# Performance work log

Measured on AMD Instinct MI355X. Metric: run time of the kernel, lower is better.

Reference implementation:

```python
import jax, jax.numpy as jnp
import numpy as np

NUM_STEPS = 3
NUM_HEADS = 8
HEAD_DIM = 128
EPS = 1e-5


def layernorm(x, g, b):
    mu = jnp.mean(x, -1, keepdims=True)
    var = jnp.mean(jnp.square(x - mu), -1, keepdims=True)
    return (x - mu) * jax.lax.rsqrt(var + EPS) * g + b


def entmax15(x):
    # Exact entmax-1.5 along last axis (Peters & Martins 2019, sort-based).
    x = (x - jnp.max(x, -1, keepdims=True)) / 2.0
    xs = jnp.flip(jnp.sort(x, -1), -1)  # descending sort
    rho = jnp.arange(1, x.shape[-1] + 1, dtype=x.dtype)
    mean = jnp.cumsum(xs, -1) / rho
    meansq = jnp.cumsum(xs * xs, -1) / rho
    ss = rho * (meansq - jnp.square(mean))
    tau = mean - jnp.sqrt(jnp.clip((1.0 - ss) / rho, 0.0, None))
    support = jnp.sum(tau <= xs, -1, keepdims=True)
    tau_star = jnp.take_along_axis(tau, support - 1, -1)
    return jnp.square(jnp.clip(x - tau_star, 0.0, None))


def setup_inputs() -> dict:
    key = jax.random.key(0)
    ks = jax.random.split(key, 6)
    B, S, Hd, Md, N = 2, 1024, 2048, 1024, 2048
    THD = NUM_HEADS * HEAD_DIM
    return {
        "hidden": jax.random.normal(ks[0], (B, S, Hd), jnp.float32),
        "memory": jax.random.normal(ks[1], (N, Md), jnp.float32),
        "Wq": jax.random.normal(ks[2], (THD, Hd), jnp.float32) / np.float32(np.sqrt(Hd)),
        "Wk": jax.random.normal(ks[3], (THD, Md), jnp.float32) / np.float32(np.sqrt(Md)),
        "Wv": jax.random.normal(ks[4], (THD, Md), jnp.float32) / np.float32(np.sqrt(Md)),
        "Wo": jax.random.normal(ks[5], (Hd, THD), jnp.float32) / np.float32(np.sqrt(THD)),
        "log_beta": jnp.full((NUM_HEADS,), float(np.log(1.0 / np.sqrt(HEAD_DIM))), jnp.float32),
        "g_state": jnp.ones((Hd,), jnp.float32),
        "b_state": jnp.zeros((Hd,), jnp.float32),
        "g_mem": jnp.ones((Md,), jnp.float32),
        "b_mem": jnp.zeros((Md,), jnp.float32),
    }


def reference(hidden, memory, Wq, Wk, Wv, Wo, log_beta, g_state, b_state, g_mem, b_mem):
    B, S, _ = hidden.shape
    N = memory.shape[0]
    H, hd = NUM_HEADS, HEAD_DIM
    # projections
    Q = layernorm(hidden, g_state, b_state) @ Wq.T            # (B,S,H*hd)
    mn = layernorm(memory, g_mem, b_mem)                      # (N,Md)
    K = (mn @ Wk.T).reshape(N, H, hd).transpose(1, 0, 2)      # (H,N,hd)
    V = (mn @ Wv.T).reshape(N, H, hd).transpose(1, 0, 2)      # (H,N,hd)
    xi = Q.reshape(B, S, H, hd).transpose(0, 2, 1, 3)          # (B,H,S,hd)
    beta = jnp.exp(log_beta)[None, :, None, None]
    for _ in range(NUM_STEPS):
        scores = jnp.einsum('bhsd,hnd->bhsn', xi, K) * beta    # (B,H,S,N)
        w = entmax15(scores)
        xi = jnp.einsum('bhsn,hnd->bhsd', w, V)
    out = xi.transpose(0, 2, 1, 3).reshape(B, S, H * hd) @ Wo.T  # (B,S,hidden_dim)
    return out
```

## Files before the change

### kernel.cpp

```cpp
#include <hip/hip_runtime.h>

typedef _Float16 half8 __attribute__((ext_vector_type(8)));
typedef _Float16 hv4 __attribute__((ext_vector_type(4)));
typedef float fv4 __attribute__((ext_vector_type(4)));

typedef __attribute__((address_space(3))) unsigned lds_u32;
typedef const __attribute__((address_space(1))) unsigned glb_u32;

__device__ __forceinline__ void gll16(const void* g, void* l) {
  __builtin_amdgcn_global_load_lds((glb_u32*)g, (lds_u32*)l, 16, 0, 0);
}

__global__ __launch_bounds__(256) void ln_rows(const float* __restrict__ in,
                                               const float* __restrict__ g,
                                               const float* __restrict__ bb,
                                               _Float16* __restrict__ out, int ncols) {
  __shared__ float sm[8];
  int row = blockIdx.x, t = threadIdx.x;
  const float* rp = in + (size_t)row * ncols;
  int nv = ncols >> 10;
  fv4 v[2];
  float s1 = 0.f, s2 = 0.f;
#pragma unroll
  for (int c = 0; c < 2; ++c)
    if (c < nv) {
      v[c] = *(const fv4*)(rp + c * 1024 + t * 4);
#pragma unroll
      for (int j = 0; j < 4; ++j) { s1 += v[c][j]; s2 += v[c][j] * v[c][j]; }
    }
#pragma unroll
  for (int off = 32; off > 0; off >>= 1) { s1 += __shfl_xor(s1, off, 64); s2 += __shfl_xor(s2, off, 64); }
  int w = t >> 6;
  if ((t & 63) == 0) { sm[w] = s1; sm[4 + w] = s2; }
  __syncthreads();
  s1 = sm[0] + sm[1] + sm[2] + sm[3];
  s2 = sm[4] + sm[5] + sm[6] + sm[7];
  float inv = 1.0f / (float)ncols;
  float mu = s1 * inv;
  float var = s2 * inv - mu * mu;
  float rstd = rsqrtf(var + 1e-5f);
#pragma unroll
  for (int c = 0; c < 2; ++c)
    if (c < nv) {
      int col = c * 1024 + t * 4;
      fv4 gg = *(const fv4*)(g + col);
      fv4 bv = *(const fv4*)(bb + col);
      hv4 o;
#pragma unroll
      for (int j = 0; j < 4; ++j) o[j] = (_Float16)(((v[c][j] - mu) * rstd) * gg[j] + bv[j]);
      *(hv4*)(out + (size_t)row * ncols + col) = o;
    }
}

__global__ __launch_bounds__(256) void cast_f16(const float* __restrict__ in,
                                                _Float16* __restrict__ out, int n) {
  int i = (blockIdx.x * 256 + threadIdx.x) << 2;
  if (i < n) {
    fv4 f = *(const fv4*)(in + i);
    hv4 h;
#pragma unroll
    for (int j = 0; j < 4; ++j) h[j] = (_Float16)f[j];
    *(hv4*)(out + i) = h;
  }
}

__global__ __launch_bounds__(256) void reduce_split(const float* __restrict__ parts, int ns,
                                                    long long stride,
                                                    _Float16* __restrict__ hi, int n) {
  int i = (blockIdx.x * 256 + threadIdx.x) << 2;
  if (i < n) {
    fv4 s = *(const fv4*)(parts + i);
    for (int j = 1; j < ns; ++j) {
      fv4 v = *(const fv4*)(parts + (size_t)j * stride + i);
      s += v;
    }
    hv4 h;
#pragma unroll
    for (int j = 0; j < 4; ++j) h[j] = (_Float16)s[j];
    *(hv4*)(hi + i) = h;
  }
}

__global__ __launch_bounds__(256) void entmax_c(const _Float16* __restrict__ scores,
                                                float* __restrict__ crow) {
  __shared__ float comp[4][512];
  int wid = threadIdx.x >> 6;
  int row = blockIdx.x * 4 + wid;
  int l = threadIdx.x & 63;
  unsigned long long lmask = (1ull << l) - 1ull;
  const half8* sp = (const half8*)(scores + (size_t)row * 2048);
  half8 hx[4];
#pragma unroll
  for (int i = 0; i < 4; ++i) hx[i] = sp[i * 64 + l];
  fv4 x[8];
#pragma unroll
  for (int i = 0; i < 4; ++i)
#pragma unroll
    for (int j = 0; j < 8; ++j) x[i * 2 + (j >> 2)][j & 3] = (float)hx[i][j];
  float m = x[0][0];
#pragma unroll
  for (int i = 0; i < 8; ++i)
#pragma unroll
    for (int j = 0; j < 4; ++j) m = fmaxf(m, x[i][j]);
#pragma unroll
  for (int off = 32; off > 0; off >>= 1) m = fmaxf(m, __shfl_xor(m, off, 64));
#pragma unroll
  for (int i = 0; i < 8; ++i)
#pragma unroll
    for (int j = 0; j < 4; ++j) x[i][j] = (x[i][j] - m) * 0.5f;

  float tau = -1.0f;
  bool fixed = false;
  int cnti = 2048;
  for (int it = 0; it < 6 && !fixed; ++it) {
    float s1 = 0.f, s2 = 0.f;
    cnti = 0;
#pragma unroll
    for (int i = 0; i < 8; ++i)
#pragma unroll
      for (int j = 0; j < 4; ++j) {
        bool a = x[i][j] > tau;
        cnti += (int)__builtin_popcountll(__ballot(a));
        float sel = a ? x[i][j] : 0.f;
        s1 += sel;
        s2 = fmaf(sel, sel, s2);
      }
#pragma unroll
    for (int off = 32; off > 0; off >>= 1) {
      s1 += __shfl_xor(s1, off, 64);
      s2 += __shfl_xor(s2, off, 64);
    }
    float cnt = (float)cnti;
    float mean = s1 / cnt;
    float ss = s2 - s1 * mean;
    float nt = mean - sqrtf(fmaxf((1.0f - ss) / cnt, 0.0f));
    if (nt == tau) fixed = true;
    else tau = nt;
    if (cnti <= 512) break;
  }
  if (!fixed) {
    if (cnti <= 512) {
      int base = 0;
#pragma unroll
      for (int i = 0; i < 8; ++i)
#pragma unroll
        for (int j = 0; j < 4; ++j) {
          bool a = x[i][j] > tau;
          unsigned long long mk = __ballot(a);
          if (a) comp[wid][base + (int)__builtin_popcountll(mk & lmask)] = x[i][j];
          base += (int)__builtin_popcountll(mk);
        }
      float y[8];
#pragma unroll
      for (int r = 0; r < 8; ++r) {
        int idx = r * 64 + l;
        y[r] = (idx < base) ? comp[wid][idx] : -2.0f;
      }
      for (int it = 0; it < 10 && !fixed; ++it) {
        float s1 = 0.f, s2 = 0.f;
        int c = 0;
#pragma unroll
        for (int r = 0; r < 8; ++r) {
          bool a = y[r] > tau;
          c += (int)__builtin_popcountll(__ballot(a));
          float sel = a ? y[r] : 0.f;
          s1 += sel;
          s2 = fmaf(sel, sel, s2);
        }
#pragma unroll
        for (int off = 32; off > 0; off >>= 1) {
          s1 += __shfl_xor(s1, off, 64);
          s2 += __shfl_xor(s2, off, 64);
        }
        float cnt = (float)c;
        float mean = s1 / cnt;
        float ss = s2 - s1 * mean;
        float nt = mean - sqrtf(fmaxf((1.0f - ss) / cnt, 0.0f));
        if (nt == tau) fixed = true;
        else tau = nt;
      }
    } else {
      for (int it = 0; it < 8 && !fixed; ++it) {
        float s1 = 0.f, s2 = 0.f;
        int c = 0;
#pragma unroll
        for (int i = 0; i < 8; ++i)
#pragma unroll
          for (int j = 0; j < 4; ++j) {
            bool a = x[i][j] > tau;
            c += (int)__builtin_popcountll(__ballot(a));
            float sel = a ? x[i][j] : 0.f;
            s1 += sel;
            s2 = fmaf(sel, sel, s2);
          }
#pragma unroll
        for (int off = 32; off > 0; off >>= 1) {
          s1 += __shfl_xor(s1, off, 64);
          s2 += __shfl_xor(s2, off, 64);
        }
        float cnt = (float)c;
        float mean = s1 / cnt;
        float ss = s2 - s1 * mean;
        float nt = mean - sqrtf(fmaxf((1.0f - ss) / cnt, 0.0f));
        if (nt == tau) fixed = true;
        else tau = nt;
      }
    }
  }

  if (l == 0) crow[row] = 0.5f * m + tau;
}

struct GemmParams {
  const _Float16 *A, *B, *B2;
  const float* crow;
  _Float16 *C16, *C16b;
  float* C32;
  const float* log_beta;
  int K, lda, ldb;
  long long aSB, aSH, bSH;
  long long crowSB, crowSH;
  long long cSB, cSH, cOsR, cOsC;
  long long cOsRb, cOsCb;
  long long partStride;
  int alphaMode, outMode, outModeB, nsplit, dual;
};

template <int AMODE>
__global__ __launch_bounds__(256) void gemm_nt(GemmParams p) {
  constexpr int AST = AMODE ? 40 : 32;
  __shared__ __align__(16) _Float16 As[128 * AST];
  __shared__ __align__(16) _Float16 Bs[128 * 32];
  int t = threadIdx.x;
  int m0 = blockIdx.y * 128;
  int bx = blockIdx.x, n0, kbeg, kend, ks = 0;
  if (p.nsplit > 1) {
    ks = bx % p.nsplit;
    n0 = (bx / p.nsplit) * 128;
    int kl = p.K / p.nsplit;
    kbeg = ks * kl;
    kend = kbeg + kl;
  } else {
    n0 = bx * 128;
    kbeg = 0;
    kend = p.K;
  }
  int z = blockIdx.z, bidx, h, job = 0;
  if (p.dual) { job = z; bidx = 0; h = 0; }
  else { bidx = z >> 3; h = z & 7; }
  const _Float16* pA = p.A + bidx * p.aSB + h * p.aSH;
  const _Float16* pB = (job ? p.B2 : p.B) + h * p.bSH;
  const float* pc = AMODE ? p.crow + bidx * p.crowSB + h * p.crowSH : nullptr;

  fv4 acc[4][4] = {};
  int wv = t >> 6, l = t & 63, quad = l >> 4, lr = l & 15;
  int wm = (wv >> 1) * 64, wn = (wv & 1) * 64;
  int rl = l >> 2, cl = (l & 3) * 8;

  for (int k0 = kbeg; k0 < kend; k0 += 32) {
#pragma unroll
    for (int v = 0; v < 2; ++v) {
      int rb = wv * 16 + v * 64;
      int r = rb + rl;
      size_t aOff = (size_t)(m0 + r) * p.lda + k0 + cl;
      size_t bOff = (size_t)(n0 + r) * p.ldb + k0 + cl;
      if (AMODE == 0) {
        gll16(pA + aOff, &As[rb * 32]);
      } else {
        half8 s8 = *(const half8*)(pA + aOff);
        _Float16 c0 = (_Float16)pc[m0 + r];
        half8 d = s8 * (_Float16)0.5f - c0;
        d = __builtin_elementwise_max(d, (half8)(0));
        half8 w8 = d * d;
        *(half8*)&As[r * AST + cl] = w8;
      }
      gll16(pB + bOff, &Bs[rb * 32]);
    }
    __syncthreads();
    half8 ah[4], bh[4];
#pragma unroll
    for (int mi = 0; mi < 4; ++mi) ah[mi] = *(const half8*)&As[(wm + mi * 16 + lr) * AST + quad * 8];
#pragma unroll
    for (int ni = 0; ni < 4; ++ni) bh[ni] = *(const half8*)&Bs[(wn + ni * 16 + lr) * 32 + quad * 8];
#pragma unroll
    for (int mi = 0; mi < 4; ++mi)
#pragma unroll
      for (int ni = 0; ni < 4; ++ni)
        acc[mi][ni] = __builtin_amdgcn_mfma_f32_16x16x32_f16(ah[mi], bh[ni], acc[mi][ni], 0, 0, 0);
    __syncthreads();
  }

  float alpha = p.alphaMode ? __expf(p.log_beta[h]) : 1.0f;
  int om = (p.dual && job) ? p.outModeB : p.outMode;
  _Float16* c16 = (p.dual && job) ? p.C16b : p.C16;
  long long osR = (p.dual && job) ? p.cOsRb : p.cOsR;
  long long osC = (p.dual && job) ? p.cOsCb : p.cOsC;
  float* c32 = p.C32 + (p.nsplit > 1 ? (long long)ks * p.partStride : 0);
  long long cOff = (long long)bidx * p.cSB + (long long)h * p.cSH;
#pragma unroll
  for (int mi = 0; mi < 4; ++mi)
#pragma unroll
    for (int ni = 0; ni < 4; ++ni) {
      int row = m0 + wm + mi * 16 + quad * 4;
      int col = n0 + wn + ni * 16 + lr;
#pragma unroll
      for (int r = 0; r < 4; ++r) {
        float val = acc[mi][ni][r] * alpha;
        long long idx = cOff + (long long)(row + r) * osR + (long long)col * osC;
        if (om == 1) c32[idx] = val;
        else c16[idx] = (_Float16)val;
      }
    }
}

extern "C" void kernel_launch(void* const* d_in, const int* in_sizes, int n_in,
                              void* d_out, int out_size, void* d_ws, size_t ws_size,
                              hipStream_t stream) {
  const float* hidden = (const float*)d_in[0];
  const float* memory = (const float*)d_in[1];
  const float* Wq = (const float*)d_in[2];
  const float* Wk = (const float*)d_in[3];
  const float* Wv = (const float*)d_in[4];
  const float* Wo = (const float*)d_in[5];
  const float* log_beta = (const float*)d_in[6];
  const float* g_state = (const float*)d_in[7];
  const float* b_state = (const float*)d_in[8];
  const float* g_mem = (const float*)d_in[9];
  const float* b_mem = (const float*)d_in[10];

  char* w = (char*)d_ws;
  auto alloc = [&](size_t bytes) {
    char* r = w;
    w += (bytes + 255) & ~(size_t)255;
    return r;
  };
  _Float16* wq16 = (_Float16*)alloc(2097152 * 2);
  _Float16* wk16 = (_Float16*)alloc(1048576 * 2);
  _Float16* wv16 = (_Float16*)alloc(1048576 * 2);
  _Float16* wo16 = (_Float16*)alloc(2097152 * 2);
  _Float16* lnh16 = (_Float16*)alloc(4194304 * 2);
  _Float16* mn16 = (_Float16*)alloc(2097152 * 2);
  _Float16* kph = (_Float16*)alloc(2097152 * 2);
  _Float16* vt16 = (_Float16*)alloc(2097152 * 2);
  _Float16* xih = (_Float16*)alloc(2097152 * 2);
  float* parts = (float*)alloc((size_t)8 * 2097152 * 4);
  _Float16* scores16 = (_Float16*)alloc((size_t)33554432 * 2);
  float* crow = (float*)alloc(16384 * 4);

  ln_rows<<<2048, 256, 0, stream>>>(hidden, g_state, b_state, lnh16, 2048);
  ln_rows<<<2048, 256, 0, stream>>>(memory, g_mem, b_mem, mn16, 1024);
  cast_f16<<<2048, 256, 0, stream>>>(Wq, wq16, 2097152);
  cast_f16<<<1024, 256, 0, stream>>>(Wk, wk16, 1048576);
  cast_f16<<<1024, 256, 0, stream>>>(Wv, wv16, 1048576);
  cast_f16<<<2048, 256, 0, stream>>>(Wo, wo16, 2097152);

  {
    GemmParams p{};
    p.A = lnh16; p.lda = 2048;
    p.B = wq16; p.ldb = 2048;
    p.K = 2048; p.nsplit = 2;
    p.C32 = parts; p.outMode = 1; p.partStride = 2097152;
    p.cOsR = 1024; p.cOsC = 1;
    gemm_nt<0><<<dim3(16, 16, 1), 256, 0, stream>>>(p);
    reduce_split<<<2048, 256, 0, stream>>>(parts, 2, 2097152, xih, 2097152);
  }
  {
    GemmParams p{};
    p.A = mn16; p.lda = 1024;
    p.B = wk16; p.B2 = wv16; p.ldb = 1024;
    p.K = 1024; p.dual = 1;
    p.C16 = kph; p.outMode = 0; p.cOsR = 1024; p.cOsC = 1;
    p.C16b = vt16; p.outModeB = 0; p.cOsRb = 1; p.cOsCb = 2048;
    gemm_nt<0><<<dim3(8, 16, 2), 256, 0, stream>>>(p);
  }

  for (int step = 0; step < 3; ++step) {
    {
      GemmParams p{};
      p.A = xih;
      p.lda = 1024; p.aSB = 1048576; p.aSH = 128;
      p.B = kph; p.ldb = 1024; p.bSH = 128;
      p.K = 128;
      p.alphaMode = 1; p.log_beta = log_beta;
      p.C16 = scores16; p.outMode = 0;
      p.cSB = 16777216; p.cSH = 2097152;
      p.cOsR = 2048; p.cOsC = 1;
      gemm_nt<0><<<dim3(16, 8, 16), 256, 0, stream>>>(p);
    }
    entmax_c<<<4096, 256, 0, stream>>>(scores16, crow);
    {
      GemmParams p{};
      p.A = scores16; p.crow = crow;
      p.lda = 2048; p.aSB = 16777216; p.aSH = 2097152;
      p.crowSB = 8192; p.crowSH = 1024;
      p.B = vt16; p.ldb = 2048; p.bSH = 262144;
      p.K = 2048; p.nsplit = 4;
      p.C32 = parts; p.outMode = 1; p.partStride = 2097152;
      p.cSB = 1048576; p.cSH = 128;
      p.cOsR = 1024; p.cOsC = 1;
      gemm_nt<1><<<dim3(4, 8, 16), 256, 0, stream>>>(p);
    }
    reduce_split<<<2048, 256, 0, stream>>>(parts, 4, 2097152, xih, 2097152);
  }

  {
    GemmParams p{};
    p.A = xih; p.lda = 1024;
    p.B = wo16; p.ldb = 1024;
    p.K = 1024;
    p.C32 = (float*)d_out; p.outMode = 1;
    p.cOsR = 2048; p.cOsC = 1;
    gemm_nt<0><<<dim3(16, 16, 1), 256, 0, stream>>>(p);
  }
}
```

Measured before the change: 478.8 us.

## Fuse scores, entmax and weighted-value GEMM into one per-step kernel

Each Hopfield step now runs as one kernel, hop_step. A block takes 16 query rows of one head, computes scaled scores with MFMA into LDS, solves the entmax threshold per row in LDS, and multiplies the entmax weights by V to write xi directly. This removes the large fp16 scores buffer in global memory and its repeated write and read, the crow buffer, the split-K partials and the reduce kernel. In exchange, every block streams the whole K and V head slices straight from global memory without LDS staging, so those loads rely heavily on cache. The roughly 74 KB of LDS per block also limits occupancy.

```diff
diff --git a/kernel.cpp b/kernel.cpp
--- a/kernel.cpp
+++ b/kernel.cpp
@@ -81,155 +81,203 @@
   }
 }
 
-__global__ __launch_bounds__(256) void entmax_c(const _Float16* __restrict__ scores,
-                                                float* __restrict__ crow) {
+#define SST 2056
+__global__ __launch_bounds__(256, 2) void hop_step(const _Float16* __restrict__ xi,
+                                                   const _Float16* __restrict__ kp,
+                                                   const _Float16* __restrict__ vt,
+                                                   const float* __restrict__ log_beta,
+                                                   _Float16* __restrict__ xout) {
+  __shared__ __align__(16) _Float16 Ss[16 * SST];
   __shared__ float comp[4][512];
-  int wid = threadIdx.x >> 6;
-  int row = blockIdx.x * 4 + wid;
-  int l = threadIdx.x & 63;
+  __shared__ float cs[16];
+  int strip = blockIdx.x, h = blockIdx.y, b = blockIdx.z;
+  int t = threadIdx.x, wv = t >> 6, l = t & 63;
+  int quad = l >> 4, lr = l & 15;
   unsigned long long lmask = (1ull << l) - 1ull;
-  const half8* sp = (const half8*)(scores + (size_t)row * 2048);
-  half8 hx[4];
-#pragma unroll
-  for (int i = 0; i < 4; ++i) hx[i] = sp[i * 64 + l];
-  fv4 x[8];
-#pragma unroll
-  for (int i = 0; i < 4; ++i)
-#pragma unroll
-    for (int j = 0; j < 8; ++j) x[i * 2 + (j >> 2)][j & 3] = (float)hx[i][j];
-  float m = x[0][0];
-#pragma unroll
-  for (int i = 0; i < 8; ++i)
-#pragma unroll
-    for (int j = 0; j < 4; ++j) m = fmaxf(m, x[i][j]);
-#pragma unroll
-  for (int off = 32; off > 0; off >>= 1) m = fmaxf(m, __shfl_xor(m, off, 64));
-#pragma unroll
-  for (int i = 0; i < 8; ++i)
-#pragma unroll
-    for (int j = 0; j < 4; ++j) x[i][j] = (x[i][j] - m) * 0.5f;
-
-  float tau = -1.0f;
-  bool fixed = false;
-  int cnti = 2048;
-  for (int it = 0; it < 6 && !fixed; ++it) {
-    float s1 = 0.f, s2 = 0.f;
-    cnti = 0;
+  float beta = __expf(log_beta[h]);
+
+  const _Float16* xiA = xi + ((size_t)(b * 1024 + strip * 16)) * 1024 + h * 128;
+  const _Float16* Kb = kp + h * 128;
+  const _Float16* Vb = vt + (size_t)h * 128 * 2048;
+
+  half8 af[4];
+#pragma unroll
+  for (int ki = 0; ki < 4; ++ki)
+    af[ki] = *(const half8*)(xiA + (size_t)lr * 1024 + ki * 32 + quad * 8);
+  for (int nt = wv * 32; nt < wv * 32 + 32; ++nt) {
+    int n0 = nt * 16;
+    fv4 acc = {};
+#pragma unroll
+    for (int ki = 0; ki < 4; ++ki) {
+      half8 bf = *(const half8*)(Kb + (size_t)(n0 + lr) * 1024 + ki * 32 + quad * 8);
+      acc = __builtin_amdgcn_mfma_f32_16x16x32_f16(af[ki], bf, acc, 0, 0, 0);
+    }
+#pragma unroll
+    for (int r = 0; r < 4; ++r)
+      Ss[(quad * 4 + r) * SST + n0 + lr] = (_Float16)(acc[r] * beta);
+  }
+  __syncthreads();
+
+  for (int rr = 0; rr < 4; ++rr) {
+    int row = wv * 4 + rr;
+    const half8* rp = (const half8*)&Ss[row * SST];
+    half8 hx[4];
+#pragma unroll
+    for (int i = 0; i < 4; ++i) hx[i] = rp[i * 64 + l];
+    fv4 x[8];
+#pragma unroll
+    for (int i = 0; i < 4; ++i)
+#pragma unroll
+      for (int j = 0; j < 8; ++j) x[i * 2 + (j >> 2)][j & 3] = (float)hx[i][j];
+    float m = x[0][0];
 #pragma unroll
     for (int i = 0; i < 8; ++i)
 #pragma unroll
-      for (int j = 0; j < 4; ++j) {
-        bool a = x[i][j] > tau;
-        cnti += (int)__builtin_popcountll(__ballot(a));
-        float sel = a ? x[i][j] : 0.f;
-        s1 += sel;
-        s2 = fmaf(sel, sel, s2);
-      }
-#pragma unroll
-    for (int off = 32; off > 0; off >>= 1) {
-      s1 += __shfl_xor(s1, off, 64);
-      s2 += __shfl_xor(s2, off, 64);
-    }
-    float cnt = (float)cnti;
-    float mean = s1 / cnt;
-    float ss = s2 - s1 * mean;
-    float nt = mean - sqrtf(fmaxf((1.0f - ss) / cnt, 0.0f));
-    if (nt == tau) fixed = true;
-    else tau = nt;
-    if (cnti <= 512) break;
-  }
-  if (!fixed) {
-    if (cnti <= 512) {
-      int base = 0;
+      for (int j = 0; j < 4; ++j) m = fmaxf(m, x[i][j]);
+#pragma unroll
+    for (int off = 32; off > 0; off >>= 1) m = fmaxf(m, __shfl_xor(m, off, 64));
+#pragma unroll
+    for (int i = 0; i < 8; ++i)
+#pragma unroll
+      for (int j = 0; j < 4; ++j) x[i][j] = (x[i][j] - m) * 0.5f;
+
+    float tau = -1.0f;
+    bool fixed = false;
+    int cnti = 2048;
+    for (int it = 0; it < 6 && !fixed; ++it) {
+      float s1 = 0.f, s2 = 0.f;
+      cnti = 0;
 #pragma unroll
       for (int i = 0; i < 8; ++i)
 #pragma unroll
         for (int j = 0; j < 4; ++j) {
           bool a = x[i][j] > tau;
-          unsigned long long mk = __ballot(a);
-          if (a) comp[wid][base + (int)__builtin_popcountll(mk & lmask)] = x[i][j];
-          base += (int)__builtin_popcountll(mk);
-        }
-      float y[8];
-#pragma unroll
-      for (int r = 0; r < 8; ++r) {
-        int idx = r * 64 + l;
-        y[r] = (idx < base) ? comp[wid][idx] : -2.0f;
-      }
-      for (int it = 0; it < 10 && !fixed; ++it) {
-        float s1 = 0.f, s2 = 0.f;
-        int c = 0;
-#pragma unroll
-        for (int r = 0; r < 8; ++r) {
-          bool a = y[r] > tau;
-          c += (int)__builtin_popcountll(__ballot(a));
-          float sel = a ? y[r] : 0.f;
+          cnti += (int)__builtin_popcountll(__ballot(a));
+          float sel = a ? x[i][j] : 0.f;
           s1 += sel;
           s2 = fmaf(sel, sel, s2);
         }
 #pragma unroll
-        for (int off = 32; off > 0; off >>= 1) {
-          s1 += __shfl_xor(s1, off, 64);
-          s2 += __shfl_xor(s2, off, 64);
-        }
-        float cnt = (float)c;
-        float mean = s1 / cnt;
-        float ss = s2 - s1 * mean;
-        float nt = mean - sqrtf(fmaxf((1.0f - ss) / cnt, 0.0f));
-        if (nt == tau) fixed = true;
-        else tau = nt;
+      for (int off = 32; off > 0; off >>= 1) {
+        s1 += __shfl_xor(s1, off, 64);
+        s2 += __shfl_xor(s2, off, 64);
       }
-    } else {
-      for (int it = 0; it < 8 && !fixed; ++it) {
-        float s1 = 0.f, s2 = 0.f;
-        int c = 0;
+      float cnt = (float)cnti;
+      float mean = s1 / cnt;
+      float ss = s2 - s1 * mean;
+      float nt = mean - sqrtf(fmaxf((1.0f - ss) / cnt, 0.0f));
+      if (nt == tau) fixed = true;
+      else tau = nt;
+      if (cnti <= 512) break;
+    }
+    if (!fixed) {
+      if (cnti <= 512) {
+        int base = 0;
 #pragma unroll
         for (int i = 0; i < 8; ++i)
 #pragma unroll
           for (int j = 0; j < 4; ++j) {
             bool a = x[i][j] > tau;
+            unsigned long long mk = __ballot(a);
+            if (a) comp[wv][base + (int)__builtin_popcountll(mk & lmask)] = x[i][j];
+            base += (int)__builtin_popcountll(mk);
+          }
+        float y[8];
+#pragma unroll
+        for (int r = 0; r < 8; ++r) {
+          int idx = r * 64 + l;
+          y[r] = (idx < base) ? comp[wv][idx] : -2.0f;
+        }
+        for (int it = 0; it < 10 && !fixed; ++it) {
+          float s1 = 0.f, s2 = 0.f;
+          int c = 0;
+#pragma unroll
+          for (int r = 0; r < 8; ++r) {
+            bool a = y[r] > tau;
             c += (int)__builtin_popcountll(__ballot(a));
-            float sel = a ? x[i][j] : 0.f;
+            float sel = a ? y[r] : 0.f;
             s1 += sel;
             s2 = fmaf(sel, sel, s2);
           }
 #pragma unroll
-        for (int off = 32; off > 0; off >>= 1) {
-          s1 += __shfl_xor(s1, off, 64);
-          s2 += __shfl_xor(s2, off, 64);
+          for (int off = 32; off > 0; off >>= 1) {
+            s1 += __shfl_xor(s1, off, 64);
+            s2 += __shfl_xor(s2, off, 64);
+          }
+          float cnt = (float)c;
+          float mean = s1 / cnt;
+          float ss = s2 - s1 * mean;
+          float nt = mean - sqrtf(fmaxf((1.0f - ss) / cnt, 0.0f));
+          if (nt == tau) fixed = true;
+          else tau = nt;
         }
-        float cnt = (float)c;
-        float mean = s1 / cnt;
-        float ss = s2 - s1 * mean;
-        float nt = mean - sqrtf(fmaxf((1.0f - ss) / cnt, 0.0f));
-        if (nt == tau) fixed = true;
-        else tau = nt;
+      } else {
+        for (int it = 0; it < 8 && !fixed; ++it) {
+          float s1 = 0.f, s2 = 0.f;
+          int c = 0;
+#pragma unroll
+          for (int i = 0; i < 8; ++i)
+#pragma unroll
+            for (int j = 0; j < 4; ++j) {
+              bool a = x[i][j] > tau;
+              c += (int)__builtin_popcountll(__ballot(a));
+              float sel = a ? x[i][j] : 0.f;
+              s1 += sel;
+              s2 = fmaf(sel, sel, s2);
+            }
+#pragma unroll
+          for (int off = 32; off > 0; off >>= 1) {
+            s1 += __shfl_xor(s1, off, 64);
+            s2 += __shfl_xor(s2, off, 64);
+          }
+          float cnt = (float)c;
+          float mean = s1 / cnt;
+          float ss = s2 - s1 * mean;
+          float nt = mean - sqrtf(fmaxf((1.0f - ss) / cnt, 0.0f));
+          if (nt == tau) fixed = true;
+          else tau = nt;
+        }
       }
     }
-  }
-
-  if (l == 0) crow[row] = 0.5f * m + tau;
+    if (l == 0) cs[row] = 0.5f * m + tau;
+  }
+  __syncthreads();
+
+  _Float16 ch = (_Float16)cs[lr];
+  fv4 acc2[2] = {{}, {}};
+  int nbase = wv * 32;
+  for (int k0 = 0; k0 < 2048; k0 += 32) {
+    half8 s8 = *(const half8*)&Ss[lr * SST + k0 + quad * 8];
+    half8 d = s8 * (_Float16)0.5f - ch;
+    d = __builtin_elementwise_max(d, (half8)(0));
+    half8 w8 = d * d;
+#pragma unroll
+    for (int ni = 0; ni < 2; ++ni) {
+      half8 bf = *(const half8*)(Vb + (size_t)(nbase + ni * 16 + lr) * 2048 + k0 + quad * 8);
+      acc2[ni] = __builtin_amdgcn_mfma_f32_16x16x32_f16(w8, bf, acc2[ni], 0, 0, 0);
+    }
+  }
+  _Float16* xo = xout + ((size_t)(b * 1024 + strip * 16)) * 1024 + h * 128;
+#pragma unroll
+  for (int ni = 0; ni < 2; ++ni)
+#pragma unroll
+    for (int r = 0; r < 4; ++r)
+      xo[(size_t)(quad * 4 + r) * 1024 + nbase + ni * 16 + lr] = (_Float16)acc2[ni][r];
 }
 
 struct GemmParams {
   const _Float16 *A, *B, *B2;
-  const float* crow;
   _Float16 *C16, *C16b;
   float* C32;
-  const float* log_beta;
   int K, lda, ldb;
-  long long aSB, aSH, bSH;
-  long long crowSB, crowSH;
-  long long cSB, cSH, cOsR, cOsC;
+  long long cOsR, cOsC;
   long long cOsRb, cOsCb;
   long long partStride;
-  int alphaMode, outMode, outModeB, nsplit, dual;
+  int outMode, outModeB, nsplit, dual;
 };
 
-template <int AMODE>
 __global__ __launch_bounds__(256) void gemm_nt(GemmParams p) {
-  constexpr int AST = AMODE ? 40 : 32;
-  __shared__ __align__(16) _Float16 As[128 * AST];
+  __shared__ __align__(16) _Float16 As[128 * 32];
   __shared__ __align__(16) _Float16 Bs[128 * 32];
   int t = threadIdx.x;
   int m0 = blockIdx.y * 128;
@@ -245,12 +293,9 @@
     kbeg = 0;
     kend = p.K;
   }
-  int z = blockIdx.z, bidx, h, job = 0;
-  if (p.dual) { job = z; bidx = 0; h = 0; }
-  else { bidx = z >> 3; h = z & 7; }
-  const _Float16* pA = p.A + bidx * p.aSB + h * p.aSH;
-  const _Float16* pB = (job ? p.B2 : p.B) + h * p.bSH;
-  const float* pc = AMODE ? p.crow + bidx * p.crowSB + h * p.crowSH : nullptr;
+  int job = p.dual ? blockIdx.z : 0;
+  const _Float16* pA = p.A;
+  const _Float16* pB = job ? p.B2 : p.B;
 
   fv4 acc[4][4] = {};
   int wv = t >> 6, l = t & 63, quad = l >> 4, lr = l & 15;
@@ -262,24 +307,13 @@
     for (int v = 0; v < 2; ++v) {
       int rb = wv * 16 + v * 64;
       int r = rb + rl;
-      size_t aOff = (size_t)(m0 + r) * p.lda + k0 + cl;
-      size_t bOff = (size_t)(n0 + r) * p.ldb + k0 + cl;
-      if (AMODE == 0) {
-        gll16(pA + aOff, &As[rb * 32]);
-      } else {
-        half8 s8 = *(const half8*)(pA + aOff);
-        _Float16 c0 = (_Float16)pc[m0 + r];
-        half8 d = s8 * (_Float16)0.5f - c0;
-        d = __builtin_elementwise_max(d, (half8)(0));
-        half8 w8 = d * d;
-        *(half8*)&As[r * AST + cl] = w8;
-      }
-      gll16(pB + bOff, &Bs[rb * 32]);
+      gll16(pA + (size_t)(m0 + r) * p.lda + k0 + cl, &As[rb * 32]);
+      gll16(pB + (size_t)(n0 + r) * p.ldb + k0 + cl, &Bs[rb * 32]);
     }
     __syncthreads();
     half8 ah[4], bh[4];
 #pragma unroll
-    for (int mi = 0; mi < 4; ++mi) ah[mi] = *(const half8*)&As[(wm + mi * 16 + lr) * AST + quad * 8];
+    for (int mi = 0; mi < 4; ++mi) ah[mi] = *(const half8*)&As[(wm + mi * 16 + lr) * 32 + quad * 8];
 #pragma unroll
     for (int ni = 0; ni < 4; ++ni) bh[ni] = *(const half8*)&Bs[(wn + ni * 16 + lr) * 32 + quad * 8];
 #pragma unroll
@@ -290,13 +324,11 @@
     __syncthreads();
   }
 
-  float alpha = p.alphaMode ? __expf(p.log_beta[h]) : 1.0f;
   int om = (p.dual && job) ? p.outModeB : p.outMode;
   _Float16* c16 = (p.dual && job) ? p.C16b : p.C16;
   long long osR = (p.dual && job) ? p.cOsRb : p.cOsR;
   long long osC = (p.dual && job) ? p.cOsCb : p.cOsC;
   float* c32 = p.C32 + (p.nsplit > 1 ? (long long)ks * p.partStride : 0);
-  long long cOff = (long long)bidx * p.cSB + (long long)h * p.cSH;
 #pragma unroll
   for (int mi = 0; mi < 4; ++mi)
 #pragma unroll
@@ -305,8 +337,8 @@
       int col = n0 + wn + ni * 16 + lr;
 #pragma unroll
       for (int r = 0; r < 4; ++r) {
-        float val = acc[mi][ni][r] * alpha;
-        long long idx = cOff + (long long)(row + r) * osR + (long long)col * osC;
+        float val = acc[mi][ni][r];
+        long long idx = (long long)(row + r) * osR + (long long)col * osC;
         if (om == 1) c32[idx] = val;
         else c16[idx] = (_Float16)val;
       }
@@ -343,9 +375,7 @@
   _Float16* kph = (_Float16*)alloc(2097152 * 2);
   _Float16* vt16 = (_Float16*)alloc(2097152 * 2);
   _Float16* xih = (_Float16*)alloc(2097152 * 2);
-  float* parts = (float*)alloc((size_t)8 * 2097152 * 4);
-  _Float16* scores16 = (_Float16*)alloc((size_t)33554432 * 2);
-  float* crow = (float*)alloc(16384 * 4);
+  float* parts = (float*)alloc((size_t)2 * 2097152 * 4);
 
   ln_rows<<<2048, 256, 0, stream>>>(hidden, g_state, b_state, lnh16, 2048);
   ln_rows<<<2048, 256, 0, stream>>>(memory, g_mem, b_mem, mn16, 1024);
@@ -361,7 +391,7 @@
     p.K = 2048; p.nsplit = 2;
     p.C32 = parts; p.outMode = 1; p.partStride = 2097152;
     p.cOsR = 1024; p.cOsC = 1;
-    gemm_nt<0><<<dim3(16, 16, 1), 256, 0, stream>>>(p);
+    gemm_nt<<<dim3(16, 16, 1), 256, 0, stream>>>(p);
     reduce_split<<<2048, 256, 0, stream>>>(parts, 2, 2097152, xih, 2097152);
   }
   {
@@ -371,37 +401,11 @@
     p.K = 1024; p.dual = 1;
     p.C16 = kph; p.outMode = 0; p.cOsR = 1024; p.cOsC = 1;
     p.C16b = vt16; p.outModeB = 0; p.cOsRb = 1; p.cOsCb = 2048;
-    gemm_nt<0><<<dim3(8, 16, 2), 256, 0, stream>>>(p);
-  }
-
-  for (int step = 0; step < 3; ++step) {
-    {
-      GemmParams p{};
-      p.A = xih;
-      p.lda = 1024; p.aSB = 1048576; p.aSH = 128;
-      p.B = kph; p.ldb = 1024; p.bSH = 128;
-      p.K = 128;
-      p.alphaMode = 1; p.log_beta = log_beta;
-      p.C16 = scores16; p.outMode = 0;
-      p.cSB = 16777216; p.cSH = 2097152;
-      p.cOsR = 2048; p.cOsC = 1;
-      gemm_nt<0><<<dim3(16, 8, 16), 256, 0, stream>>>(p);
-    }
-    entmax_c<<<4096, 256, 0, stream>>>(scores16, crow);
-    {
-      GemmParams p{};
-      p.A = scores16; p.crow = crow;
-      p.lda = 2048; p.aSB = 16777216; p.aSH = 2097152;
-      p.crowSB = 8192; p.crowSH = 1024;
-      p.B = vt16; p.ldb = 2048; p.bSH = 262144;
-      p.K = 2048; p.nsplit = 4;
-      p.C32 = parts; p.outMode = 1; p.partStride = 2097152;
-      p.cSB = 1048576; p.cSH = 128;
-      p.cOsR = 1024; p.cOsC = 1;
-      gemm_nt<1><<<dim3(4, 8, 16), 256, 0, stream>>>(p);
-    }
-    reduce_split<<<2048, 256, 0, stream>>>(parts, 4, 2097152, xih, 2097152);
-  }
+    gemm_nt<<<dim3(8, 16, 2), 256, 0, stream>>>(p);
+  }
+
+  for (int step = 0; step < 3; ++step)
+    hop_step<<<dim3(64, 8, 2), 256, 0, stream>>>(xih, kph, vt16, log_beta, xih);
 
   {
     GemmParams p{};
@@ -410,6 +414,6 @@
     p.K = 1024;
     p.C32 = (float*)d_out; p.outMode = 1;
     p.cOsR = 2048; p.cOsC = 1;
-    gemm_nt<0><<<dim3(16, 16, 1), 256, 0, stream>>>(p);
-  }
-}
+    gemm_nt<<<dim3(16, 16, 1), 256, 0, stream>>>(p);
+  }
+}
```

Measured after the change: 615.3 us. 28.5% more time.
